# Kernel tuning notes

Measured on AMD Instinct MI355X. Metric: run time of the kernel, lower is better.

## Reference

```python
import jax, jax.numpy as jnp
import numpy as np

DEPTH, HEADS, DIM, DIM_HEAD, MLP = 2, 8, 512, 64, 2048
INNER = HEADS * DIM_HEAD  # == DIM here, but project_out is still True since dim_head != dim
NEG = -1e9


def _ln(t, g, b):
    mu = t.mean(-1, keepdims=True)
    var = ((t - mu) ** 2).mean(-1, keepdims=True)
    return (t - mu) / jnp.sqrt(var + 1e-5) * g + b


def _heads(t):
    b, n, hd = t.shape
    return t.reshape(b, n, HEADS, hd // HEADS).transpose(0, 2, 1, 3)  # b h n d


def _merge(t):
    b, h, n, d = t.shape
    return t.transpose(0, 2, 1, 3).reshape(b, n, h * d)


def kat_forward(x, kx, rd, clst, mask, kmask,
                ln1_g, ln1_b, Wqkv, Wout, bout, ln2_g, ln2_b, W1, b1, W2, b2):
    scale = DIM_HEAD ** -0.5
    # att_mask[b,1,n,m]: True where attention is disallowed (mask_i * kmask_j < 0.5)
    att_mask = (jnp.einsum('bid,bjd->bij', mask, kmask) < 0.5)[:, None]
    krd = rd[:, None]                      # [b,1,m,n]
    krdT = jnp.swapaxes(krd, -1, -2)       # [b,1,n,m]
    keep = (kmask >= 0.5)                  # kernel_mask fill-with-0 complement
    k_reps, atten = [], []
    for l in range(DEPTH):
        # pre-norm applied in-place before residual (as in the original)
        xn = _ln(x, ln1_g[l], ln1_b[l])
        kxn = _ln(kx, ln1_g[l], ln1_b[l])
        cn = _ln(clst, ln1_g[l], ln1_b[l])

        def qkv(t):
            q, k, v = jnp.split(t @ Wqkv[l], 3, axis=-1)
            return _heads(q), _heads(k), _heads(v)

        tq, tk, tv = qkv(xn)
        kq, kk, kv = qkv(kxn)
        cq, _, _ = qkv(cn)

        # patch -> kernel attention, krd-weighted dual softmax
        dots = jnp.einsum('bhid,bhjd->bhij', tq, kk) * scale      # [b,h,n,m]
        dots = jnp.where(att_mask, NEG, dots)
        attn_t = jax.nn.softmax(dots * 24, -1) * krdT             # temperature branch (attention map out)
        attn = jax.nn.softmax(dots, -1) * krdT
        x_ = _merge(jnp.einsum('bhij,bhjd->bhid', attn, kv)) @ Wout[l] + bout[l]

        # kernel -> patch attention
        kd = jnp.einsum('bhid,bhjd->bhij', kq, tk) * scale        # [b,h,m,n]
        kd = jnp.where(jnp.swapaxes(att_mask, -1, -2), NEG, kd)
        kattn = jax.nn.softmax(kd, -1) * krd
        kx_ = _merge(jnp.einsum('bhij,bhjd->bhid', kattn, tv)) @ Wout[l] + bout[l]

        # class token -> kernel attention
        cd = jnp.einsum('bhid,bhjd->bhij', cq, kk) * scale        # [b,h,1,m]
        cd = jnp.where(att_mask[:, :, :1], NEG, cd)
        c_ = _merge(jnp.einsum('bhij,bhjd->bhid', jax.nn.softmax(cd, -1), kv)) @ Wout[l] + bout[l]

        x, kx, clst = xn + x_, kxn + kx_, cn + c_

        def ff(t):
            tn = _ln(t, ln2_g[l], ln2_b[l])
            return jax.nn.gelu(tn @ W1[l] + b1[l], approximate=False) @ W2[l] + b2[l]

        x, kx, clst = ff(x) + x, ff(kx) + kx, ff(clst) + clst
        k_reps.append(kx * keep)
        atten.append(jnp.swapaxes(attn_t, -1, -2))  # [b,h,m,n]
    return jnp.stack(k_reps), clst, jnp.stack(atten)


def setup_inputs() -> dict:
    key = jax.random.key(0)
    ks = jax.random.split(key, 16)
    b, n, m = 4, 2048, 256
    s = 0.02
    L = DEPTH
    return {
        'x': jax.random.normal(ks[0], (b, n, DIM), jnp.float32),
        'kx': jax.random.normal(ks[1], (b, m, DIM), jnp.float32),
        'rd': jax.random.uniform(ks[2], (b, m, n), jnp.float32),
        'clst': jax.random.normal(ks[3], (b, 1, DIM), jnp.float32),
        'mask': jnp.ones((b, n, 1), jnp.float32),
        'kmask': jax.random.uniform(ks[4], (b, m, 1), jnp.float32),
        'ln1_g': jnp.ones((L, DIM), jnp.float32),
        'ln1_b': jnp.zeros((L, DIM), jnp.float32),
        'Wqkv': s * jax.random.normal(ks[5], (L, DIM, 3 * INNER), jnp.float32),
        'Wout': s * jax.random.normal(ks[6], (L, INNER, DIM), jnp.float32),
        'bout': jnp.zeros((L, DIM), jnp.float32),
        'ln2_g': jnp.ones((L, DIM), jnp.float32),
        'ln2_b': jnp.zeros((L, DIM), jnp.float32),
        'W1': s * jax.random.normal(ks[7], (L, DIM, MLP), jnp.float32),
        'b1': jnp.zeros((L, MLP), jnp.float32),
        'W2': s * jax.random.normal(ks[8], (L, MLP, DIM), jnp.float32),
        'b2': jnp.zeros((L, DIM), jnp.float32),
    }


def reference(x, kx, rd, clst, mask, kmask, ln1_g, ln1_b, Wqkv, Wout, bout,
              ln2_g, ln2_b, W1, b1, W2, b2):
    return kat_forward(x, kx, rd, clst, mask, kmask, ln1_g, ln1_b, Wqkv, Wout,
                       bout, ln2_g, ln2_b, W1, b1, W2, b2)
```

## Files before the change

kernel.cpp:

```cpp
#include <hip/hip_runtime.h>
#include <hip/hip_bf16.h>
#include <cstddef>

#define DEV __device__ __forceinline__

constexpr int Bb  = 4;
constexpr int Nn  = 2048;
constexpr int MK  = 256;
constexpr int Dd  = 512;
constexpr int Hh  = 8;
constexpr int DH  = 64;
constexpr int QLD = 1536;
constexpr int MLPD = 2048;
constexpr int NTOK = Bb * Nn + Bb * MK + Bb;
constexpr int KXOFF = Bb * Nn;
constexpr int CLOFF = Bb * Nn + Bb * MK;
constexpr float SCALE = 0.125f;
constexpr float NEGV  = -1e9f;

typedef __attribute__((ext_vector_type(8))) short short8;
typedef __attribute__((ext_vector_type(4))) float f32x4;

DEV float4 ldf4(const float* p) { return *reinterpret_cast<const float4*>(p); }

DEV void gload16(const short* g, short* l) {
  __builtin_amdgcn_global_load_lds(
      (const __attribute__((address_space(1))) void*)g,
      (__attribute__((address_space(3))) void*)l, 16, 0, 0);
}

DEV float waveMax(float v) {
#pragma unroll
  for (int o = 32; o; o >>= 1) v = fmaxf(v, __shfl_xor(v, o));
  return v;
}
DEV float waveSum(float v) {
#pragma unroll
  for (int o = 32; o; o >>= 1) v += __shfl_xor(v, o);
  return v;
}
DEV float blockMax256(float v, float* red) {
  v = waveMax(v);
  __syncthreads();
  if ((threadIdx.x & 63) == 0) red[threadIdx.x >> 6] = v;
  __syncthreads();
  return fmaxf(fmaxf(red[0], red[1]), fmaxf(red[2], red[3]));
}
DEV float blockSum256(float v, float* red) {
  v = waveSum(v);
  __syncthreads();
  if ((threadIdx.x & 63) == 0) red[threadIdx.x >> 6] = v;
  __syncthreads();
  return red[0] + red[1] + red[2] + red[3];
}
DEV float gelu_f(float x) { return 0.5f * x * (1.f + erff(x * 0.70710678118654752f)); }
DEV float pow24(float e1) {
  float e2 = e1 * e1, e4 = e2 * e2, e8 = e4 * e4, e16 = e8 * e8;
  return e16 * e8;
}

__global__ __launch_bounds__(256)
void copy3_kernel(const float* __restrict__ x, const float* __restrict__ kx,
                  const float* __restrict__ c, float* __restrict__ dst) {
  const int idx = blockIdx.x * 256 + threadIdx.x;
  const int row = idx >> 7;
  float4 v;
  if (row < KXOFF) v = ldf4(x + (size_t)idx * 4);
  else if (row < CLOFF) v = ldf4(kx + (size_t)idx * 4 - (size_t)KXOFF * Dd);
  else v = ldf4(c + (size_t)idx * 4 - (size_t)CLOFF * Dd);
  *reinterpret_cast<float4*>(dst + (size_t)idx * 4) = v;
}

__global__ __launch_bounds__(64)
void ln_kernel(const float* __restrict__ in, const float* __restrict__ gw,
               const float* __restrict__ bw, __hip_bfloat16* __restrict__ outb) {
  const int row = blockIdx.x;
  const int t = threadIdx.x;
  const float* p = in + (size_t)row * Dd + t * 8;
  float4 v0 = ldf4(p), v1 = ldf4(p + 4);
  float s = v0.x + v0.y + v0.z + v0.w + v1.x + v1.y + v1.z + v1.w;
  float q = v0.x*v0.x + v0.y*v0.y + v0.z*v0.z + v0.w*v0.w
          + v1.x*v1.x + v1.y*v1.y + v1.z*v1.z + v1.w*v1.w;
  s = waveSum(s); q = waveSum(q);
  const float mu = s * (1.f / Dd);
  const float rstd = rsqrtf(fmaxf(q * (1.f / Dd) - mu * mu, 0.f) + 1e-5f);
  float4 g0 = ldf4(gw + t * 8), g1 = ldf4(gw + t * 8 + 4);
  float4 b0 = ldf4(bw + t * 8), b1 = ldf4(bw + t * 8 + 4);
  float o[8];
  o[0] = (v0.x - mu) * rstd * g0.x + b0.x;
  o[1] = (v0.y - mu) * rstd * g0.y + b0.y;
  o[2] = (v0.z - mu) * rstd * g0.z + b0.z;
  o[3] = (v0.w - mu) * rstd * g0.w + b0.w;
  o[4] = (v1.x - mu) * rstd * g1.x + b1.x;
  o[5] = (v1.y - mu) * rstd * g1.y + b1.y;
  o[6] = (v1.z - mu) * rstd * g1.z + b1.z;
  o[7] = (v1.w - mu) * rstd * g1.w + b1.w;
  __hip_bfloat16* ob = outb + (size_t)row * Dd + t * 8;
#pragma unroll
  for (int e = 0; e < 8; ++e) ob[e] = __float2bfloat16(o[e]);
}

struct GArgs {
  const short* A;  long asb; int lda;
  const short* Bt; long bsb; int ldb;
  float* C; __hip_bfloat16* Cb;
  long czo, czi; int ldc;
  const float* bias;
  const float* res; const __hip_bfloat16* resb; int ldr;
  int M, N, K;
};

template<int BM, int BN, int EPI>
__global__ __launch_bounds__(256)
void mgemm(GArgs g) {
  constexpr int WMW = (BN >= 128) ? 2 : 4;
  constexpr int WNW = 4 / WMW;
  constexpr int WM = BM / WMW, WN = BN / WNW;
  constexpr int FM = WM / 16, FN = WN / 16;
  __shared__ __align__(16) short As[BM * 64];
  __shared__ __align__(16) short Bs[BN * 64];
  const int tid = threadIdx.x, l = tid & 63, w = tid >> 6;
  const int wm = (WNW == 2) ? (w >> 1) : w;
  const int wn = (WNW == 2) ? (w & 1) : 0;
  int bx = blockIdx.x, by = blockIdx.y;
  {
    const int gx = gridDim.x, nwg = gx * gridDim.y;
    const int orig = by * gx + bx;
    const int xcd = orig & 7, pos = orig >> 3;
    const int q = nwg >> 3, rmd = nwg & 7;
    const int s = (xcd < rmd ? xcd * (q + 1) : rmd * (q + 1) + (xcd - rmd) * q) + pos;
    bx = s % gx; by = s / gx;
  }
  const int z = blockIdx.z;
  const short* Ab = g.A + (size_t)z * g.asb;
  const short* Bb_ = g.Bt + (size_t)z * g.bsb;
  f32x4 acc[FM][FN] = {};
  const int lr = l & 15, lg = l >> 4;

  for (int k0 = 0; k0 < g.K; k0 += 64) {
    __syncthreads();
#pragma unroll
    for (int it = 0; it < BM / 32; ++it) {
      int idx = tid + it * 256, r = idx >> 3, c = idx & 7;
      int gm = by * BM + r;
      if (gm >= g.M) gm = g.M - 1;
      gload16(Ab + (size_t)gm * g.lda + k0 + ((c ^ (r & 7)) * 8), As + idx * 8);
    }
#pragma unroll
    for (int it = 0; it < BN / 32; ++it) {
      int idx = tid + it * 256, r = idx >> 3, c = idx & 7;
      int gn = bx * BN + r;
      gload16(Bb_ + (size_t)gn * g.ldb + k0 + ((c ^ (r & 7)) * 8), Bs + idx * 8);
    }
    __syncthreads();
#pragma unroll
    for (int ks = 0; ks < 2; ++ks) {
      short8 a[FM], b[FN];
#pragma unroll
      for (int fm = 0; fm < FM; ++fm) {
        int rr = wm * WM + fm * 16 + lr;
        int ch = (ks * 4 + lg) ^ (rr & 7);
        a[fm] = *reinterpret_cast<const short8*>(As + rr * 64 + ch * 8);
      }
#pragma unroll
      for (int fn = 0; fn < FN; ++fn) {
        int rn = wn * WN + fn * 16 + lr;
        int ch = (ks * 4 + lg) ^ (rn & 7);
        b[fn] = *reinterpret_cast<const short8*>(Bs + rn * 64 + ch * 8);
      }
#pragma unroll
      for (int fm = 0; fm < FM; ++fm)
#pragma unroll
        for (int fn = 0; fn < FN; ++fn)
          acc[fm][fn] = __builtin_amdgcn_mfma_f32_16x16x32_bf16(a[fm], b[fn], acc[fm][fn], 0, 0, 0);
    }
  }

  const size_t zoff = (size_t)(z >> 3) * g.czo + (size_t)(z & 7) * g.czi;
#pragma unroll
  for (int fm = 0; fm < FM; ++fm) {
#pragma unroll
    for (int fn = 0; fn < FN; ++fn) {
#pragma unroll
      for (int r = 0; r < 4; ++r) {
        int m = by * BM + wm * WM + fm * 16 + lg * 4 + r;
        int n = bx * BN + wn * WN + fn * 16 + lr;
        if (m >= g.M) continue;
        float v = acc[fm][fn][r];
        size_t coff = zoff + (size_t)m * g.ldc + n;
        if (EPI == 0) {
          g.C[coff] = v;
        } else if (EPI == 2) {
          v += g.bias[n] + g.res[(size_t)m * g.ldr + n];
          g.C[coff] = v;
        } else if (EPI == 5) {
          v += g.bias[n] + __bfloat162float(g.resb[(size_t)m * g.ldr + n]);
          g.C[coff] = v;
        } else if (EPI == 3) {
          v = gelu_f(v + g.bias[n]);
          g.Cb[coff] = __float2bfloat16(v);
        } else {
          g.Cb[coff] = __float2bfloat16(v);
        }
      }
    }
  }
}

template<int BM, int BN, int EPI>
static void launch_mgemm(const GArgs& g, int zdim, hipStream_t s) {
  dim3 grid((g.N + BN - 1) / BN, (g.M + BM - 1) / BM, zdim);
  mgemm<BM, BN, EPI><<<grid, 256, 0, s>>>(g);
}

__global__ __launch_bounds__(256)
void prep_attn_kernel(const float* __restrict__ qkv_x, const float* __restrict__ qkv_k,
                      __hip_bfloat16* __restrict__ tq_s, __hip_bfloat16* __restrict__ tk_hi,
                      __hip_bfloat16* __restrict__ kq_hi, __hip_bfloat16* __restrict__ kk_s,
                      __hip_bfloat16* __restrict__ tvT, __hip_bfloat16* __restrict__ kvT) {
  __shared__ float t[64][65];
  const int blk = blockIdx.x, tid = threadIdx.x;
  if (blk < 4096 + 512) {
    const bool isX = blk < 4096;
    const int T = isX ? Nn : MK;
    const float* qkv = isX ? qkv_x : qkv_k;
    const int idx = (isX ? blk : blk - 4096) * 256 + tid;
    const int token = idx >> 7, c8 = (idx & 127) * 8;
    const int b = token / T, i = token - b * T;
    const float* p = qkv + (size_t)token * QLD + c8;
    float v[8];
    float4 a = ldf4(p), c = ldf4(p + 4);
    v[0]=a.x; v[1]=a.y; v[2]=a.z; v[3]=a.w; v[4]=c.x; v[5]=c.y; v[6]=c.z; v[7]=c.w;
    if (c8 < 512) {
      int h = c8 >> 6, d = c8 & 63;
      if (isX) {
        __hip_bfloat16* q = tq_s + ((size_t)((b * 8 + h) * T + i)) * 128 + d;
#pragma unroll
        for (int e = 0; e < 8; ++e) {
          __hip_bfloat16 hi = __float2bfloat16(v[e]);
          q[e] = hi;
          q[64 + e] = __float2bfloat16(v[e] - __bfloat162float(hi));
        }
      } else {
        __hip_bfloat16* q = kq_hi + ((size_t)((b * 8 + h) * T + i)) * 64 + d;
#pragma unroll
        for (int e = 0; e < 8; ++e) q[e] = __float2bfloat16(v[e]);
      }
    } else {
      int cc = c8 - 512, h = cc >> 6, d = cc & 63;
      if (isX) {
        __hip_bfloat16* k = tk_hi + ((size_t)((b * 8 + h) * T + i)) * 64 + d;
#pragma unroll
        for (int e = 0; e < 8; ++e) k[e] = __float2bfloat16(v[e]);
      } else {
        __hip_bfloat16* k = kk_s + ((size_t)((b * 8 + h) * T + i)) * 128 + d;
#pragma unroll
        for (int e = 0; e < 8; ++e) {
          __hip_bfloat16 hi = __float2bfloat16(v[e]);
          k[e] = hi;
          k[64 + e] = __float2bfloat16(v[e] - __bfloat162float(hi));
        }
      }
    }
    return;
  }
  const bool isX = blk < 5632;
  const int r = isX ? blk - 4608 : blk - 5632;
  const int T = isX ? Nn : MK;
  const int tilesPerBh = T / 64;
  const int bh = r / tilesPerBh, i0 = (r % tilesPerBh) * 64;
  const int b = bh >> 3, h = bh & 7;
  const float* qkv = isX ? qkv_x : qkv_k;
  __hip_bfloat16* vT = isX ? tvT : kvT;
#pragma unroll
  for (int it = 0; it < 4; ++it) {
    int idx = tid + it * 256, rr = idx >> 4, f = idx & 15;
    float4 v = ldf4(qkv + (size_t)(b * T + i0 + rr) * QLD + 2 * Dd + h * 64 + f * 4);
    t[rr][f * 4 + 0] = v.x; t[rr][f * 4 + 1] = v.y;
    t[rr][f * 4 + 2] = v.z; t[rr][f * 4 + 3] = v.w;
  }
  __syncthreads();
#pragma unroll
  for (int it = 0; it < 4; ++it) {
    int idx = tid + it * 256, d = idx >> 4, c4 = (idx & 15) * 4;
    __hip_bfloat16* op = vT + (size_t)(bh * 64 + d) * T + i0 + c4;
#pragma unroll
    for (int e = 0; e < 4; ++e) op[e] = __float2bfloat16(t[c4 + e][d]);
  }
}

__global__ __launch_bounds__(512)
void score_sx_kernel(const short* __restrict__ Q, const short* __restrict__ Km,
                     const float* __restrict__ mask, const float* __restrict__ kmask,
                     const float* __restrict__ rdT,
                     __hip_bfloat16* __restrict__ P1, float* __restrict__ atten) {
  __shared__ __align__(16) char smem[49152];
  short* As = (short*)smem;
  short* Bs = (short*)(smem + 16384);
  float* tb = (float*)smem;
  __shared__ float red[128 * 2];
  __shared__ float red2[128 * 4];
  const int tid = threadIdx.x, l = tid & 63, w = tid >> 6;
  const int wm = w >> 1, wn = w & 1;
  const int by = blockIdx.x, bh = blockIdx.y;
  const int b = bh >> 3;
  const short* Ab = Q + (size_t)bh * Nn * 128;
  const short* Bb = Km + (size_t)bh * MK * 128;
  const int lr = l & 15, lg = l >> 4;
  f32x4 acc[2][8] = {};

  for (int k0 = 0; k0 < 128; k0 += 64) {
    __syncthreads();
#pragma unroll
    for (int it = 0; it < 2; ++it) {
      int idx = tid + it * 512, r = idx >> 3, c = idx & 7;
      gload16(Ab + (size_t)(by * 128 + r) * 128 + k0 + ((c ^ (r & 7)) * 8), As + idx * 8);
    }
#pragma unroll
    for (int it = 0; it < 4; ++it) {
      int idx = tid + it * 512, r = idx >> 3, c = idx & 7;
      gload16(Bb + (size_t)r * 128 + k0 + ((c ^ (r & 7)) * 8), Bs + idx * 8);
    }
    __syncthreads();
#pragma unroll
    for (int ks = 0; ks < 2; ++ks) {
      short8 a[2], bv[8];
#pragma unroll
      for (int fm = 0; fm < 2; ++fm) {
        int rr = wm * 32 + fm * 16 + lr;
        int ch = (ks * 4 + lg) ^ (rr & 7);
        a[fm] = *reinterpret_cast<const short8*>(As + rr * 64 + ch * 8);
      }
#pragma unroll
      for (int fn = 0; fn < 8; ++fn) {
        int rn = wn * 128 + fn * 16 + lr;
        int ch = (ks * 4 + lg) ^ (rn & 7);
        bv[fn] = *reinterpret_cast<const short8*>(Bs + rn * 64 + ch * 8);
      }
#pragma unroll
      for (int fm = 0; fm < 2; ++fm)
#pragma unroll
        for (int fn = 0; fn < 8; ++fn)
          acc[fm][fn] = __builtin_amdgcn_mfma_f32_16x16x32_bf16(a[fm], bv[fn], acc[fm][fn], 0, 0, 0);
    }
  }
  {
    float colm[8];
#pragma unroll
    for (int fn = 0; fn < 8; ++fn)
      colm[fn] = kmask[b * MK + wn * 128 + fn * 16 + lr];
#pragma unroll
    for (int fm = 0; fm < 2; ++fm)
#pragma unroll
      for (int r = 0; r < 4; ++r) {
        float rm = mask[(size_t)b * Nn + by * 128 + wm * 32 + fm * 16 + lg * 4 + r];
#pragma unroll
        for (int fn = 0; fn < 8; ++fn)
          acc[fm][fn][r] = (rm * colm[fn] < 0.5f) ? NEGV : acc[fm][fn][r] * SCALE;
      }
  }
  float mx[2][4];
#pragma unroll
  for (int fm = 0; fm < 2; ++fm)
#pragma unroll
    for (int r = 0; r < 4; ++r) {
      float m = -3.4e38f;
#pragma unroll
      for (int fn = 0; fn < 8; ++fn) m = fmaxf(m, acc[fm][fn][r]);
#pragma unroll
      for (int o = 8; o; o >>= 1) m = fmaxf(m, __shfl_xor(m, o));
      mx[fm][r] = m;
    }
  __syncthreads();
  if (lr == 0) {
#pragma unroll
    for (int fm = 0; fm < 2; ++fm)
#pragma unroll
      for (int r = 0; r < 4; ++r)
        red[(wm * 32 + fm * 16 + lg * 4 + r) * 2 + wn] = mx[fm][r];
  }
  __syncthreads();
#pragma unroll
  for (int fm = 0; fm < 2; ++fm)
#pragma unroll
    for (int r = 0; r < 4; ++r) {
      int row = wm * 32 + fm * 16 + lg * 4 + r;
      mx[fm][r] = fmaxf(red[row * 2], red[row * 2 + 1]);
    }
  float s1[2][4], s24[2][4];
#pragma unroll
  for (int fm = 0; fm < 2; ++fm)
#pragma unroll
    for (int r = 0; r < 4; ++r) {
      float a1 = 0.f, a24 = 0.f;
#pragma unroll
      for (int fn = 0; fn < 8; ++fn) {
        float e1 = __expf(acc[fm][fn][r] - mx[fm][r]);
        acc[fm][fn][r] = e1;
        a1 += e1;
        a24 += pow24(e1);
      }
#pragma unroll
      for (int o = 8; o; o >>= 1) { a1 += __shfl_xor(a1, o); a24 += __shfl_xor(a24, o); }
      s1[fm][r] = a1; s24[fm][r] = a24;
    }
  __syncthreads();
  if (lr == 0) {
#pragma unroll
    for (int fm = 0; fm < 2; ++fm)
#pragma unroll
      for (int r = 0; r < 4; ++r) {
        int row = wm * 32 + fm * 16 + lg * 4 + r;
        red2[row * 4 + wn * 2]     = s1[fm][r];
        red2[row * 4 + wn * 2 + 1] = s24[fm][r];
      }
  }
  __syncthreads();
#pragma unroll
  for (int fm = 0; fm < 2; ++fm)
#pragma unroll
    for (int r = 0; r < 4; ++r) {
      int row = wm * 32 + fm * 16 + lg * 4 + r;
      s1[fm][r]  = 1.f / (red2[row * 4] + red2[row * 4 + 2]);
      s24[fm][r] = 1.f / (red2[row * 4 + 1] + red2[row * 4 + 3]);
    }
#pragma unroll
  for (int fm = 0; fm < 2; ++fm) {
#pragma unroll
    for (int r = 0; r < 4; ++r) {
      int m = by * 128 + wm * 32 + fm * 16 + lg * 4 + r;
      const float* rp = rdT + ((size_t)b * Nn + m) * MK;
      size_t obase = ((size_t)bh * Nn + m) * MK;
#pragma unroll
      for (int fn = 0; fn < 8; ++fn) {
        int n = wn * 128 + fn * 16 + lr;
        float e1 = acc[fm][fn][r];
        float rv = rp[n];
        P1[obase + n] = __float2bfloat16(e1 * s1[fm][r] * rv);
        acc[fm][fn][r] = pow24(e1) * s24[fm][r] * rv;
      }
    }
  }
  const int jw = tid >> 1, ipw = (tid & 1) * 16;
#pragma unroll
  for (int c = 0; c < 4; ++c) {
    __syncthreads();
    if (wm == c) {
#pragma unroll
      for (int fm = 0; fm < 2; ++fm)
#pragma unroll
        for (int r = 0; r < 4; ++r) {
          int mloc = fm * 16 + lg * 4 + r;
#pragma unroll
          for (int fn = 0; fn < 8; ++fn) {
            int n = wn * 128 + fn * 16 + lr;
            tb[n * 33 + mloc] = acc[fm][fn][r];
          }
        }
    }
    __syncthreads();
    float* op = atten + ((size_t)bh * MK + jw) * Nn + by * 128 + c * 32 + ipw;
    const float* tp = tb + jw * 33 + ipw;
#pragma unroll
    for (int e = 0; e < 4; ++e)
      *reinterpret_cast<float4*>(op + e * 4) =
          make_float4(tp[e * 4], tp[e * 4 + 1], tp[e * 4 + 2], tp[e * 4 + 3]);
  }
}

__global__ __launch_bounds__(256)
void score_sk_kernel(const short* __restrict__ Qk, const short* __restrict__ Kt,
                     const float* __restrict__ mask, const float* __restrict__ kmask,
                     const float* __restrict__ rd, __hip_bfloat16* __restrict__ P2) {
  __shared__ __align__(16) short As[16 * 64];
  __shared__ __align__(16) short Bs[256 * 64];
  __shared__ float redm[16 * 4];
  __shared__ float reds[16 * 4];
  const int tid = threadIdx.x, l = tid & 63, w = tid >> 6;
  const int lr = l & 15, lg = l >> 4;
  const int bh = blockIdx.x, j0 = blockIdx.y * 16, b = bh >> 3;
  const short* Ab = Qk + ((size_t)bh * MK + j0) * 64;
  const short* Bb = Kt + (size_t)bh * Nn * 64;
  f32x4 acc[32];
#pragma unroll
  for (int q = 0; q < 32; ++q) acc[q] = f32x4{0.f, 0.f, 0.f, 0.f};
  if (tid < 128) {
    int r = tid >> 3, c = tid & 7;
    gload16(Ab + (size_t)r * 64 + ((c ^ (r & 7)) * 8), As + tid * 8);
  }
#pragma unroll
  for (int nc = 0; nc < 8; ++nc) {
    __syncthreads();
#pragma unroll
    for (int it = 0; it < 8; ++it) {
      int idx = tid + it * 256, r = idx >> 3, c = idx & 7;
      gload16(Bb + (size_t)(nc * 256 + r) * 64 + ((c ^ (r & 7)) * 8), Bs + idx * 8);
    }
    __syncthreads();
#pragma unroll
    for (int ks = 0; ks < 2; ++ks) {
      short8 a;
      {
        int ch = (ks * 4 + lg) ^ (lr & 7);
        a = *reinterpret_cast<const short8*>(As + lr * 64 + ch * 8);
      }
#pragma unroll
      for (int fn = 0; fn < 4; ++fn) {
        int rn = w * 64 + fn * 16 + lr;
        int ch = (ks * 4 + lg) ^ (rn & 7);
        short8 bv = *reinterpret_cast<const short8*>(Bs + rn * 64 + ch * 8);
        acc[nc * 4 + fn] =
            __builtin_amdgcn_mfma_f32_16x16x32_bf16(a, bv, acc[nc * 4 + fn], 0, 0, 0);
      }
    }
  }
  float rm[4];
#pragma unroll
  for (int rr = 0; rr < 4; ++rr) rm[rr] = kmask[b * MK + j0 + lg * 4 + rr];
  float mx[4] = {-3.4e38f, -3.4e38f, -3.4e38f, -3.4e38f};
#pragma unroll
  for (int q = 0; q < 32; ++q) {
    int n = (q >> 2) * 256 + w * 64 + (q & 3) * 16 + lr;
    float cm = mask[(size_t)b * Nn + n];
#pragma unroll
    for (int rr = 0; rr < 4; ++rr) {
      float v = (rm[rr] * cm < 0.5f) ? NEGV : acc[q][rr] * SCALE;
      acc[q][rr] = v;
      mx[rr] = fmaxf(mx[rr], v);
    }
  }
#pragma unroll
  for (int o = 8; o; o >>= 1)
#pragma unroll
    for (int rr = 0; rr < 4; ++rr) mx[rr] = fmaxf(mx[rr], __shfl_xor(mx[rr], o));
  __syncthreads();
  if (lr == 0) {
#pragma unroll
    for (int rr = 0; rr < 4; ++rr) redm[(lg * 4 + rr) * 4 + w] = mx[rr];
  }
  __syncthreads();
#pragma unroll
  for (int rr = 0; rr < 4; ++rr) {
    int row = lg * 4 + rr;
    mx[rr] = fmaxf(fmaxf(redm[row * 4], redm[row * 4 + 1]),
                   fmaxf(redm[row * 4 + 2], redm[row * 4 + 3]));
  }
  float sm[4] = {0.f, 0.f, 0.f, 0.f};
#pragma unroll
  for (int q = 0; q < 32; ++q)
#pragma unroll
    for (int rr = 0; rr < 4; ++rr) {
      float e = __expf(acc[q][rr] - mx[rr]);
      acc[q][rr] = e;
      sm[rr] += e;
    }
#pragma unroll
  for (int o = 8; o; o >>= 1)
#pragma unroll
    for (int rr = 0; rr < 4; ++rr) sm[rr] += __shfl_xor(sm[rr], o);
  __syncthreads();
  if (lr == 0) {
#pragma unroll
    for (int rr = 0; rr < 4; ++rr) reds[(lg * 4 + rr) * 4 + w] = sm[rr];
  }
  __syncthreads();
  float inv[4];
#pragma unroll
  for (int rr = 0; rr < 4; ++rr) {
    int row = lg * 4 + rr;
    inv[rr] = 1.f / (reds[row * 4] + reds[row * 4 + 1] + reds[row * 4 + 2] + reds[row * 4 + 3]);
  }
#pragma unroll
  for (int rr = 0; rr < 4; ++rr) {
    int j = j0 + lg * 4 + rr;
    const float* rp = rd + (size_t)(b * MK + j) * Nn;
    __hip_bfloat16* pp = P2 + ((size_t)bh * MK + j) * Nn;
#pragma unroll
    for (int q = 0; q < 32; ++q) {
      int n = (q >> 2) * 256 + w * 64 + (q & 3) * 16 + lr;
      pp[n] = __float2bfloat16(acc[q][rr] * inv[rr] * rp[n]);
    }
  }
}

__global__ __launch_bounds__(256)
void rd_tr_kernel(const float* __restrict__ rd, float* __restrict__ rdT) {
  __shared__ float tb[64][65];
  const int b = blockIdx.x;
  const int i0 = blockIdx.y * 64, j0 = blockIdx.z * 64;
  const int tid = threadIdx.x;
#pragma unroll
  for (int it = 0; it < 4; ++it) {
    int idx = tid + it * 256, r = idx >> 4, c4 = (idx & 15) * 4;
    float4 v = ldf4(rd + ((size_t)(b * MK + j0 + r)) * Nn + i0 + c4);
    tb[r][c4 + 0] = v.x; tb[r][c4 + 1] = v.y; tb[r][c4 + 2] = v.z; tb[r][c4 + 3] = v.w;
  }
  __syncthreads();
#pragma unroll
  for (int it = 0; it < 4; ++it) {
    int idx = tid + it * 256, r = idx >> 4, c4 = (idx & 15) * 4;
    float4 o = make_float4(tb[c4 + 0][r], tb[c4 + 1][r], tb[c4 + 2][r], tb[c4 + 3][r]);
    *reinterpret_cast<float4*>(rdT + ((size_t)(b * Nn + i0 + r)) * MK + j0 + c4) = o;
  }
}

struct WtArgs {
  const float* W[8];
  __hip_bfloat16* T[8];
  int K[8], N[8];
};
__global__ __launch_bounds__(256)
void wtrans_all_kernel(WtArgs a) {
  __shared__ float t[64][65];
  const int e = blockIdx.z;
  const int K = a.K[e], N = a.N[e];
  const int n0 = blockIdx.x * 64, k0 = blockIdx.y * 64;
  if (n0 >= N || k0 >= K) return;
  const float* W = a.W[e];
  __hip_bfloat16* WT = a.T[e];
  const int tid = threadIdx.x;
#pragma unroll
  for (int it = 0; it < 4; ++it) {
    int idx = tid + it * 256, r = idx >> 4, f = idx & 15;
    float4 v = ldf4(W + (size_t)(k0 + r) * N + n0 + f * 4);
    t[r][f * 4 + 0] = v.x; t[r][f * 4 + 1] = v.y;
    t[r][f * 4 + 2] = v.z; t[r][f * 4 + 3] = v.w;
  }
  __syncthreads();
#pragma unroll
  for (int it = 0; it < 4; ++it) {
    int idx = tid + it * 256, r = idx >> 4, c4 = (idx & 15) * 4;
    __hip_bfloat16* op = WT + (size_t)(n0 + r) * K + k0 + c4;
#pragma unroll
    for (int e2 = 0; e2 < 4; ++e2) op[e2] = __float2bfloat16(t[c4 + e2][r]);
  }
}

__global__ __launch_bounds__(256)
void attn_c_kernel(const float* __restrict__ cqkv, const float* __restrict__ kqkv,
                   const float* __restrict__ mask, const float* __restrict__ kmask,
                   __hip_bfloat16* __restrict__ c_pre) {
  __shared__ __align__(16) float kv_s[MK][DH];
  __shared__ __align__(16) float q_s[DH];
  __shared__ float pbuf[MK];
  __shared__ float red8[8];
  __shared__ float redpv[4][DH];
  const int tid = threadIdx.x;
  const int bh = blockIdx.x, b = bh >> 3, h = bh & 7;
  const float* vp = kqkv + ((size_t)(b * MK + tid)) * QLD + 2 * Dd + h * DH;
#pragma unroll
  for (int q4 = 0; q4 < 16; ++q4)
    *reinterpret_cast<float4*>(&kv_s[tid][q4 * 4]) = ldf4(vp + q4 * 4);
  if (tid < DH) q_s[tid] = cqkv[(size_t)b * QLD + h * DH + tid];
  __syncthreads();
  const float* kp = kqkv + ((size_t)(b * MK + tid)) * QLD + Dd + h * DH;
  float dot = 0.f;
#pragma unroll
  for (int q4 = 0; q4 < 16; ++q4) {
    float4 kv4 = ldf4(kp + q4 * 4);
    float4 qv = ldf4(&q_s[q4 * 4]);
    dot = fmaf(qv.x, kv4.x, dot);
    dot = fmaf(qv.y, kv4.y, dot);
    dot = fmaf(qv.z, kv4.z, dot);
    dot = fmaf(qv.w, kv4.w, dot);
  }
  const float dm = (mask[(size_t)b * Nn] * kmask[b * MK + tid] < 0.5f) ? NEGV : dot * SCALE;
  const float mx = blockMax256(dm, red8);
  const float e = __expf(dm - mx);
  const float s = blockSum256(e, red8);
  pbuf[tid] = e / s;
  __syncthreads();
  const int d = tid & 63, g = tid >> 6;
  float acc = 0.f;
#pragma unroll 8
  for (int jj = 0; jj < 64; ++jj)
    acc = fmaf(pbuf[g * 64 + jj], kv_s[g * 64 + jj][d], acc);
  redpv[g][d] = acc;
  __syncthreads();
  if (tid < DH)
    c_pre[(size_t)b * Dd + h * DH + tid] = __float2bfloat16(
        redpv[0][tid] + redpv[1][tid] + redpv[2][tid] + redpv[3][tid]);
}

__global__ void kreps_kernel(const float* __restrict__ kx, const float* __restrict__ kmask,
                             float* __restrict__ o) {
  const int idx = blockIdx.x * 256 + threadIdx.x;
  const int bj = idx >> 9;
  const float keep = (kmask[bj] >= 0.5f) ? 1.f : 0.f;
  o[idx] = kx[idx] * keep;
}
__global__ void cout_kernel(const float* __restrict__ c_s, float* __restrict__ o) {
  const int idx = blockIdx.x * 256 + threadIdx.x;
  o[idx] = c_s[idx];
}

static GArgs ga_base() { GArgs g = {}; return g; }

extern "C" void kernel_launch(void* const* d_in, const int* in_sizes, int n_in,
                              void* d_out, int out_size, void* d_ws, size_t ws_size,
                              hipStream_t stream) {
  (void)in_sizes; (void)n_in; (void)out_size; (void)ws_size;
  const float* x_in  = (const float*)d_in[0];
  const float* kx_in = (const float*)d_in[1];
  const float* rd    = (const float*)d_in[2];
  const float* c_in  = (const float*)d_in[3];
  const float* mask  = (const float*)d_in[4];
  const float* kmask = (const float*)d_in[5];
  const float* ln1g  = (const float*)d_in[6];
  const float* ln1b  = (const float*)d_in[7];
  const float* Wqkv  = (const float*)d_in[8];
  const float* Woutw = (const float*)d_in[9];
  const float* boutw = (const float*)d_in[10];
  const float* ln2g  = (const float*)d_in[11];
  const float* ln2b  = (const float*)d_in[12];
  const float* W1    = (const float*)d_in[13];
  const float* b1    = (const float*)d_in[14];
  const float* W2    = (const float*)d_in[15];
  const float* b2    = (const float*)d_in[16];
  float* out = (float*)d_out;

  float* ws = (float*)d_ws;
  size_t off = 0;
  auto alloc = [&](size_t n) { float* p = ws + off; off += (n + 15) & ~(size_t)15; return p; };
  float* xcat_s    = alloc((size_t)NTOK * Dd);
  float* xcat_nb_f = alloc((size_t)NTOK * Dd / 2);
  float* pre_cat_f = alloc((size_t)NTOK * Dd / 2);
  float* qkv       = alloc((size_t)NTOK * QLD);
  float* P1_f      = alloc((size_t)32 * Nn * MK / 2);
  float* P2_f      = alloc((size_t)32 * MK * Nn / 2);
  float* tq_s_f    = alloc((size_t)32 * Nn * 128 / 2);
  float* kk_s_f    = alloc((size_t)32 * MK * 128 / 2);
  float* tk_hi_f   = alloc((size_t)32 * Nn * 64 / 2);
  float* kq_hi_f   = alloc((size_t)32 * MK * 64 / 2);
  float* tvT_f     = alloc((size_t)32 * 64 * Nn / 2);
  float* kvT_f     = alloc((size_t)32 * 64 * MK / 2);
  float* rdT       = alloc((size_t)Bb * Nn * MK);
  float* WqkvT_f   = alloc((size_t)2 * QLD * Dd / 2);
  float* WoutT_f   = alloc((size_t)2 * Dd * Dd / 2);
  float* W1T_f     = alloc((size_t)2 * MLPD * Dd / 2);
  float* W2T_f     = alloc((size_t)2 * Dd * MLPD / 2);

  __hip_bfloat16* xcat_nb = (__hip_bfloat16*)xcat_nb_f;
  __hip_bfloat16* pre_cat = (__hip_bfloat16*)pre_cat_f;
  __hip_bfloat16* P1b     = (__hip_bfloat16*)P1_f;
  __hip_bfloat16* P2b     = (__hip_bfloat16*)P2_f;
  __hip_bfloat16* tq_s    = (__hip_bfloat16*)tq_s_f;
  __hip_bfloat16* kk_s    = (__hip_bfloat16*)kk_s_f;
  __hip_bfloat16* tk_hi   = (__hip_bfloat16*)tk_hi_f;
  __hip_bfloat16* kq_hi   = (__hip_bfloat16*)kq_hi_f;
  __hip_bfloat16* tvT     = (__hip_bfloat16*)tvT_f;
  __hip_bfloat16* kvT     = (__hip_bfloat16*)kvT_f;
  __hip_bfloat16* WqkvT   = (__hip_bfloat16*)WqkvT_f;
  __hip_bfloat16* WoutT   = (__hip_bfloat16*)WoutT_f;
  __hip_bfloat16* W1T     = (__hip_bfloat16*)W1T_f;
  __hip_bfloat16* W2T     = (__hip_bfloat16*)W2T_f;
  __hip_bfloat16* hid     = (__hip_bfloat16*)qkv;

  const size_t CL_OFF = (size_t)2 * Bb * MK * Dd;
  const size_t AT_OFF = CL_OFF + (size_t)Bb * Dd;

  copy3_kernel<<<(NTOK * 128) / 256, 256, 0, stream>>>(x_in, kx_in, c_in, xcat_s);
  rd_tr_kernel<<<dim3(Bb, Nn / 64, MK / 64), 256, 0, stream>>>(rd, rdT);
  {
    WtArgs a;
    for (int l = 0; l < 2; ++l) {
      a.W[l * 4 + 0] = Wqkv + (size_t)l * Dd * QLD;  a.T[l * 4 + 0] = WqkvT + (size_t)l * QLD * Dd;
      a.K[l * 4 + 0] = Dd;   a.N[l * 4 + 0] = QLD;
      a.W[l * 4 + 1] = Woutw + (size_t)l * Dd * Dd;  a.T[l * 4 + 1] = WoutT + (size_t)l * Dd * Dd;
      a.K[l * 4 + 1] = Dd;   a.N[l * 4 + 1] = Dd;
      a.W[l * 4 + 2] = W1 + (size_t)l * Dd * MLPD;   a.T[l * 4 + 2] = W1T + (size_t)l * MLPD * Dd;
      a.K[l * 4 + 2] = Dd;   a.N[l * 4 + 2] = MLPD;
      a.W[l * 4 + 3] = W2 + (size_t)l * MLPD * Dd;   a.T[l * 4 + 3] = W2T + (size_t)l * Dd * MLPD;
      a.K[l * 4 + 3] = MLPD; a.N[l * 4 + 3] = Dd;
    }
    wtrans_all_kernel<<<dim3(32, 32, 8), 256, 0, stream>>>(a);
  }

  for (int l = 0; l < 2; ++l) {
    const float* bo  = boutw + (size_t)l * Dd;
    const float* b1l = b1 + (size_t)l * MLPD;
    const float* b2l = b2 + (size_t)l * Dd;
    __hip_bfloat16* WqkvTl = WqkvT + (size_t)l * QLD * Dd;
    __hip_bfloat16* WoutTl = WoutT + (size_t)l * Dd * Dd;
    __hip_bfloat16* W1Tl   = W1T + (size_t)l * MLPD * Dd;
    __hip_bfloat16* W2Tl   = W2T + (size_t)l * Dd * MLPD;

    ln_kernel<<<NTOK, 64, 0, stream>>>(xcat_s, ln1g + l * Dd, ln1b + l * Dd, xcat_nb);

    {
      GArgs g = ga_base();
      g.A = (const short*)xcat_nb; g.lda = Dd;
      g.Bt = (const short*)WqkvTl; g.ldb = Dd;
      g.C = qkv; g.ldc = QLD;
      g.M = NTOK; g.N = QLD; g.K = Dd;
      launch_mgemm<128, 128, 0>(g, 1, stream);
    }

    prep_attn_kernel<<<5760, 256, 0, stream>>>(
        qkv, qkv + (size_t)KXOFF * QLD, tq_s, tk_hi, kq_hi, kk_s, tvT, kvT);

    attn_c_kernel<<<Bb * Hh, 256, 0, stream>>>(qkv + (size_t)CLOFF * QLD,
                                               qkv + (size_t)KXOFF * QLD, mask, kmask,
                                               pre_cat + (size_t)CLOFF * Dd);

    score_sx_kernel<<<dim3(Nn / 128, 32), 512, 0, stream>>>(
        (const short*)tq_s, (const short*)kk_s, mask, kmask, rdT, P1b,
        out + AT_OFF + (size_t)l * 32 * MK * Nn);
    {
      GArgs g = ga_base();
      g.A = (const short*)P1b; g.asb = (long)Nn * MK; g.lda = MK;
      g.Bt = (const short*)kvT; g.bsb = (long)64 * MK; g.ldb = MK;
      g.Cb = pre_cat; g.czo = (long)Nn * Dd; g.czi = 64; g.ldc = Dd;
      g.M = Nn; g.N = 64; g.K = MK;
      launch_mgemm<128, 64, 4>(g, 32, stream);
    }
    score_sk_kernel<<<dim3(32, MK / 16), 256, 0, stream>>>(
        (const short*)kq_hi, (const short*)tk_hi, mask, kmask, rd, P2b);
    {
      GArgs g = ga_base();
      g.A = (const short*)P2b; g.asb = (long)MK * Nn; g.lda = Nn;
      g.Bt = (const short*)tvT; g.bsb = (long)64 * Nn; g.ldb = Nn;
      g.Cb = pre_cat + (size_t)KXOFF * Dd; g.czo = (long)MK * Dd; g.czi = 64; g.ldc = Dd;
      g.M = MK; g.N = 64; g.K = Nn;
      launch_mgemm<64, 64, 4>(g, 32, stream);
    }

    {
      GArgs g = ga_base();
      g.A = (const short*)pre_cat; g.lda = Dd;
      g.Bt = (const short*)WoutTl; g.ldb = Dd;
      g.C = xcat_s; g.ldc = Dd; g.bias = bo; g.resb = xcat_nb; g.ldr = Dd;
      g.M = NTOK; g.N = Dd; g.K = Dd;
      launch_mgemm<128, 64, 5>(g, 1, stream);
    }

    ln_kernel<<<NTOK, 64, 0, stream>>>(xcat_s, ln2g + l * Dd, ln2b + l * Dd, xcat_nb);
    {
      GArgs g = ga_base();
      g.A = (const short*)xcat_nb; g.lda = Dd;
      g.Bt = (const short*)W1Tl; g.ldb = Dd;
      g.Cb = hid; g.ldc = MLPD; g.bias = b1l;
      g.M = NTOK; g.N = MLPD; g.K = Dd;
      launch_mgemm<128, 128, 3>(g, 1, stream);
      GArgs h = ga_base();
      h.A = (const short*)hid; h.lda = MLPD;
      h.Bt = (const short*)W2Tl; h.ldb = MLPD;
      h.C = xcat_s; h.ldc = Dd; h.bias = b2l; h.res = xcat_s; h.ldr = Dd;
      h.M = NTOK; h.N = Dd; h.K = MLPD;
      launch_mgemm<128, 64, 2>(h, 1, stream);
    }

    kreps_kernel<<<(Bb * MK * Dd) / 256, 256, 0, stream>>>(
        xcat_s + (size_t)KXOFF * Dd, kmask, out + (size_t)l * Bb * MK * Dd);
  }
  cout_kernel<<<(Bb * Dd) / 256, 256, 0, stream>>>(xcat_s + (size_t)CLOFF * Dd, out + CL_OFF);
}
```

Baseline: 687.9 us.

## Fuse QKV projection with attention-layout scatter and fold kernel-rep output into MLP epilogue

Replaces the generic QKV GEMM plus separate prep_attn relayout kernel with a dedicated GEMM whose epilogue writes bf16 hi/lo split Q/K, transposed V via shared memory, and the class-token query directly. This avoids writing and rereading the full fp32 qkv buffer. The class-token attention now reads the bf16 split K and transposed V. The masked kernel-rep output is produced in the W2 GEMM epilogue instead of a separate kernel. The cost is scattered epilogue stores and slightly different precision on the class-token path.

New measurement: 653.2 us, median of 2. -5.1%, faster.

```diff
diff --git a/kernel.cpp b/kernel.cpp
--- a/kernel.cpp
+++ b/kernel.cpp
@@ -57,6 +57,10 @@
 DEV float pow24(float e1) {
   float e2 = e1 * e1, e4 = e2 * e2, e8 = e4 * e4, e16 = e8 * e8;
   return e16 * e8;
+}
+DEV short bf16bits(float v) {
+  __hip_bfloat16 h = __float2bfloat16(v);
+  return *reinterpret_cast<short*>(&h);
 }
 
 __global__ __launch_bounds__(256)
@@ -107,6 +111,7 @@
   long czo, czi; int ldc;
   const float* bias;
   const float* res; const __hip_bfloat16* resb; int ldr;
+  float* out2; const float* km2;
   int M, N, K;
 };
 
@@ -196,6 +201,14 @@
         } else if (EPI == 5) {
           v += g.bias[n] + __bfloat162float(g.resb[(size_t)m * g.ldr + n]);
           g.C[coff] = v;
+        } else if (EPI == 6) {
+          v += g.bias[n] + g.res[(size_t)m * g.ldr + n];
+          g.C[coff] = v;
+          if (m >= KXOFF && m < CLOFF) {
+            int t = m - KXOFF;
+            float keep = (g.km2[t] >= 0.5f) ? 1.f : 0.f;
+            g.out2[(size_t)t * Dd + n] = v * keep;
+          }
         } else if (EPI == 3) {
           v = gelu_f(v + g.bias[n]);
           g.Cb[coff] = __float2bfloat16(v);
@@ -213,79 +226,159 @@
   mgemm<BM, BN, EPI><<<grid, 256, 0, s>>>(g);
 }
 
+struct QArgs {
+  const short* A; int lda;
+  const short* Bt; int ldb;
+  __hip_bfloat16 *tq, *tk, *kq, *kk, *tvT, *kvT;
+  float* cq;
+  int M, K;
+};
+
 __global__ __launch_bounds__(256)
-void prep_attn_kernel(const float* __restrict__ qkv_x, const float* __restrict__ qkv_k,
-                      __hip_bfloat16* __restrict__ tq_s, __hip_bfloat16* __restrict__ tk_hi,
-                      __hip_bfloat16* __restrict__ kq_hi, __hip_bfloat16* __restrict__ kk_s,
-                      __hip_bfloat16* __restrict__ tvT, __hip_bfloat16* __restrict__ kvT) {
-  __shared__ float t[64][65];
-  const int blk = blockIdx.x, tid = threadIdx.x;
-  if (blk < 4096 + 512) {
-    const bool isX = blk < 4096;
-    const int T = isX ? Nn : MK;
-    const float* qkv = isX ? qkv_x : qkv_k;
-    const int idx = (isX ? blk : blk - 4096) * 256 + tid;
-    const int token = idx >> 7, c8 = (idx & 127) * 8;
-    const int b = token / T, i = token - b * T;
-    const float* p = qkv + (size_t)token * QLD + c8;
-    float v[8];
-    float4 a = ldf4(p), c = ldf4(p + 4);
-    v[0]=a.x; v[1]=a.y; v[2]=a.z; v[3]=a.w; v[4]=c.x; v[5]=c.y; v[6]=c.z; v[7]=c.w;
-    if (c8 < 512) {
-      int h = c8 >> 6, d = c8 & 63;
-      if (isX) {
-        __hip_bfloat16* q = tq_s + ((size_t)((b * 8 + h) * T + i)) * 128 + d;
-#pragma unroll
-        for (int e = 0; e < 8; ++e) {
-          __hip_bfloat16 hi = __float2bfloat16(v[e]);
-          q[e] = hi;
-          q[64 + e] = __float2bfloat16(v[e] - __bfloat162float(hi));
+void qkv_gemm(QArgs g) {
+  __shared__ __align__(16) char smem[34816];
+  short* As = (short*)smem;
+  short* Bs = (short*)(smem + 16384);
+  short* tb = (short*)smem;
+  const int tid = threadIdx.x, l = tid & 63, w = tid >> 6;
+  const int wm = w >> 1, wn = w & 1;
+  int bx = blockIdx.x, by = blockIdx.y;
+  {
+    const int gx = gridDim.x, nwg = gx * gridDim.y;
+    const int orig = by * gx + bx;
+    const int xcd = orig & 7, pos = orig >> 3;
+    const int q = nwg >> 3, rmd = nwg & 7;
+    const int s = (xcd < rmd ? xcd * (q + 1) : rmd * (q + 1) + (xcd - rmd) * q) + pos;
+    bx = s % gx; by = s / gx;
+  }
+  f32x4 acc[4][4] = {};
+  const int lr = l & 15, lg = l >> 4;
+
+  for (int k0 = 0; k0 < g.K; k0 += 64) {
+    __syncthreads();
+#pragma unroll
+    for (int it = 0; it < 4; ++it) {
+      int idx = tid + it * 256, r = idx >> 3, c = idx & 7;
+      int gm = by * 128 + r;
+      if (gm >= g.M) gm = g.M - 1;
+      gload16(g.A + (size_t)gm * g.lda + k0 + ((c ^ (r & 7)) * 8), As + idx * 8);
+    }
+#pragma unroll
+    for (int it = 0; it < 4; ++it) {
+      int idx = tid + it * 256, r = idx >> 3, c = idx & 7;
+      int gn = bx * 128 + r;
+      gload16(g.Bt + (size_t)gn * g.ldb + k0 + ((c ^ (r & 7)) * 8), Bs + idx * 8);
+    }
+    __syncthreads();
+#pragma unroll
+    for (int ks = 0; ks < 2; ++ks) {
+      short8 a[4], b[4];
+#pragma unroll
+      for (int fm = 0; fm < 4; ++fm) {
+        int rr = wm * 64 + fm * 16 + lr;
+        int ch = (ks * 4 + lg) ^ (rr & 7);
+        a[fm] = *reinterpret_cast<const short8*>(As + rr * 64 + ch * 8);
+      }
+#pragma unroll
+      for (int fn = 0; fn < 4; ++fn) {
+        int rn = wn * 64 + fn * 16 + lr;
+        int ch = (ks * 4 + lg) ^ (rn & 7);
+        b[fn] = *reinterpret_cast<const short8*>(Bs + rn * 64 + ch * 8);
+      }
+#pragma unroll
+      for (int fm = 0; fm < 4; ++fm)
+#pragma unroll
+        for (int fn = 0; fn < 4; ++fn)
+          acc[fm][fn] = __builtin_amdgcn_mfma_f32_16x16x32_bf16(a[fm], b[fn], acc[fm][fn], 0, 0, 0);
+    }
+  }
+
+  const int sec = bx >> 2;
+  const int region = (by < 64) ? 0 : (by < 72 ? 1 : 2);
+
+  if (sec == 2) {
+    if (region == 2) return;
+    __syncthreads();
+#pragma unroll
+    for (int fm = 0; fm < 4; ++fm)
+#pragma unroll
+      for (int fn = 0; fn < 4; ++fn)
+#pragma unroll
+        for (int r = 0; r < 4; ++r) {
+          int mloc = wm * 64 + fm * 16 + lg * 4 + r;
+          int nloc = wn * 64 + fn * 16 + lr;
+          tb[nloc * 136 + mloc] = bf16bits(acc[fm][fn][r]);
         }
-      } else {
-        __hip_bfloat16* q = kq_hi + ((size_t)((b * 8 + h) * T + i)) * 64 + d;
-#pragma unroll
-        for (int e = 0; e < 8; ++e) q[e] = __float2bfloat16(v[e]);
-      }
+    __syncthreads();
+    const int nloc = tid >> 1, mh = (tid & 1) * 64;
+    const int nv = (bx - 8) * 128 + nloc;
+    const int h = nv >> 6, d = nv & 63;
+    int T, b, ibase;
+    __hip_bfloat16* vT;
+    if (region == 0) {
+      T = Nn; b = by >> 4; ibase = (by & 15) * 128 + mh; vT = g.tvT;
     } else {
-      int cc = c8 - 512, h = cc >> 6, d = cc & 63;
-      if (isX) {
-        __hip_bfloat16* k = tk_hi + ((size_t)((b * 8 + h) * T + i)) * 64 + d;
-#pragma unroll
-        for (int e = 0; e < 8; ++e) k[e] = __float2bfloat16(v[e]);
-      } else {
-        __hip_bfloat16* k = kk_s + ((size_t)((b * 8 + h) * T + i)) * 128 + d;
-#pragma unroll
-        for (int e = 0; e < 8; ++e) {
-          __hip_bfloat16 hi = __float2bfloat16(v[e]);
-          k[e] = hi;
-          k[64 + e] = __float2bfloat16(v[e] - __bfloat162float(hi));
+      T = MK; int t0 = (by - 64) * 128 + mh; b = t0 >> 8; ibase = t0 & 255; vT = g.kvT;
+    }
+    short* dst = (short*)vT + ((size_t)(b * 8 + h) * 64 + d) * T + ibase;
+    const short* src = tb + nloc * 136 + mh;
+#pragma unroll
+    for (int e = 0; e < 8; ++e)
+      *reinterpret_cast<short8*>(dst + e * 8) = *reinterpret_cast<const short8*>(src + e * 8);
+    return;
+  }
+
+  if (region == 2) {
+    if (sec == 0) {
+#pragma unroll
+      for (int fm = 0; fm < 4; ++fm)
+#pragma unroll
+        for (int fn = 0; fn < 4; ++fn)
+#pragma unroll
+          for (int r = 0; r < 4; ++r) {
+            int m = by * 128 + wm * 64 + fm * 16 + lg * 4 + r;
+            if (m >= g.M) continue;
+            int n = bx * 128 + wn * 64 + fn * 16 + lr;
+            g.cq[(size_t)(m - CLOFF) * Dd + n] = acc[fm][fn][r];
+          }
+    }
+    return;
+  }
+
+  const int T = region ? MK : Nn;
+#pragma unroll
+  for (int fm = 0; fm < 4; ++fm) {
+#pragma unroll
+    for (int fn = 0; fn < 4; ++fn) {
+#pragma unroll
+      for (int r = 0; r < 4; ++r) {
+        int m = by * 128 + wm * 64 + fm * 16 + lg * 4 + r;
+        int n = bx * 128 + wn * 64 + fn * 16 + lr;
+        float v = acc[fm][fn][r];
+        int t = region ? m - KXOFF : m;
+        int b = region ? (t >> 8) : (t >> 11);
+        int i = region ? (t & 255) : (t & 2047);
+        int h = (n >> 6) & 7, d = n & 63;
+        size_t tok = (size_t)(b * 8 + h) * T + i;
+        if (sec == 0) {
+          if (region == 0) {
+            __hip_bfloat16 hi = __float2bfloat16(v);
+            g.tq[tok * 128 + d] = hi;
+            g.tq[tok * 128 + 64 + d] = __float2bfloat16(v - __bfloat162float(hi));
+          } else {
+            g.kq[tok * 64 + d] = __float2bfloat16(v);
+          }
+        } else {
+          if (region == 0) {
+            g.tk[tok * 64 + d] = __float2bfloat16(v);
+          } else {
+            __hip_bfloat16 hi = __float2bfloat16(v);
+            g.kk[tok * 128 + d] = hi;
+            g.kk[tok * 128 + 64 + d] = __float2bfloat16(v - __bfloat162float(hi));
+          }
         }
       }
     }
-    return;
-  }
-  const bool isX = blk < 5632;
-  const int r = isX ? blk - 4608 : blk - 5632;
-  const int T = isX ? Nn : MK;
-  const int tilesPerBh = T / 64;
-  const int bh = r / tilesPerBh, i0 = (r % tilesPerBh) * 64;
-  const int b = bh >> 3, h = bh & 7;
-  const float* qkv = isX ? qkv_x : qkv_k;
-  __hip_bfloat16* vT = isX ? tvT : kvT;
-#pragma unroll
-  for (int it = 0; it < 4; ++it) {
-    int idx = tid + it * 256, rr = idx >> 4, f = idx & 15;
-    float4 v = ldf4(qkv + (size_t)(b * T + i0 + rr) * QLD + 2 * Dd + h * 64 + f * 4);
-    t[rr][f * 4 + 0] = v.x; t[rr][f * 4 + 1] = v.y;
-    t[rr][f * 4 + 2] = v.z; t[rr][f * 4 + 3] = v.w;
-  }
-  __syncthreads();
-#pragma unroll
-  for (int it = 0; it < 4; ++it) {
-    int idx = tid + it * 256, d = idx >> 4, c4 = (idx & 15) * 4;
-    __hip_bfloat16* op = vT + (size_t)(bh * 64 + d) * T + i0 + c4;
-#pragma unroll
-    for (int e = 0; e < 4; ++e) op[e] = __float2bfloat16(t[c4 + e][d]);
   }
 }
 
@@ -637,7 +730,8 @@
 }
 
 __global__ __launch_bounds__(256)
-void attn_c_kernel(const float* __restrict__ cqkv, const float* __restrict__ kqkv,
+void attn_c_kernel(const float* __restrict__ cq, const __hip_bfloat16* __restrict__ kk,
+                   const __hip_bfloat16* __restrict__ kvT,
                    const float* __restrict__ mask, const float* __restrict__ kmask,
                    __hip_bfloat16* __restrict__ c_pre) {
   __shared__ __align__(16) float kv_s[MK][DH];
@@ -647,22 +741,17 @@
   __shared__ float redpv[4][DH];
   const int tid = threadIdx.x;
   const int bh = blockIdx.x, b = bh >> 3, h = bh & 7;
-  const float* vp = kqkv + ((size_t)(b * MK + tid)) * QLD + 2 * Dd + h * DH;
-#pragma unroll
-  for (int q4 = 0; q4 < 16; ++q4)
-    *reinterpret_cast<float4*>(&kv_s[tid][q4 * 4]) = ldf4(vp + q4 * 4);
-  if (tid < DH) q_s[tid] = cqkv[(size_t)b * QLD + h * DH + tid];
-  __syncthreads();
-  const float* kp = kqkv + ((size_t)(b * MK + tid)) * QLD + Dd + h * DH;
+#pragma unroll
+  for (int d = 0; d < DH; ++d)
+    kv_s[tid][d] = __bfloat162float(kvT[((size_t)(b * 8 + h) * 64 + d) * MK + tid]);
+  if (tid < DH) q_s[tid] = cq[(size_t)b * Dd + h * DH + tid];
+  __syncthreads();
+  const __hip_bfloat16* kp = kk + ((size_t)((b * 8 + h) * MK + tid)) * 128;
   float dot = 0.f;
 #pragma unroll
-  for (int q4 = 0; q4 < 16; ++q4) {
-    float4 kv4 = ldf4(kp + q4 * 4);
-    float4 qv = ldf4(&q_s[q4 * 4]);
-    dot = fmaf(qv.x, kv4.x, dot);
-    dot = fmaf(qv.y, kv4.y, dot);
-    dot = fmaf(qv.z, kv4.z, dot);
-    dot = fmaf(qv.w, kv4.w, dot);
+  for (int d = 0; d < DH; ++d) {
+    float kd = __bfloat162float(kp[d]) + __bfloat162float(kp[64 + d]);
+    dot = fmaf(q_s[d], kd, dot);
   }
   const float dm = (mask[(size_t)b * Nn] * kmask[b * MK + tid] < 0.5f) ? NEGV : dot * SCALE;
   const float mx = blockMax256(dm, red8);
@@ -682,13 +771,6 @@
         redpv[0][tid] + redpv[1][tid] + redpv[2][tid] + redpv[3][tid]);
 }
 
-__global__ void kreps_kernel(const float* __restrict__ kx, const float* __restrict__ kmask,
-                             float* __restrict__ o) {
-  const int idx = blockIdx.x * 256 + threadIdx.x;
-  const int bj = idx >> 9;
-  const float keep = (kmask[bj] >= 0.5f) ? 1.f : 0.f;
-  o[idx] = kx[idx] * keep;
-}
 __global__ void cout_kernel(const float* __restrict__ c_s, float* __restrict__ o) {
   const int idx = blockIdx.x * 256 + threadIdx.x;
   o[idx] = c_s[idx];
@@ -725,7 +807,8 @@
   float* xcat_s    = alloc((size_t)NTOK * Dd);
   float* xcat_nb_f = alloc((size_t)NTOK * Dd / 2);
   float* pre_cat_f = alloc((size_t)NTOK * Dd / 2);
-  float* qkv       = alloc((size_t)NTOK * QLD);
+  float* hid_f     = alloc((size_t)NTOK * MLPD / 2);
+  float* cq        = alloc((size_t)Bb * Dd);
   float* P1_f      = alloc((size_t)32 * Nn * MK / 2);
   float* P2_f      = alloc((size_t)32 * MK * Nn / 2);
   float* tq_s_f    = alloc((size_t)32 * Nn * 128 / 2);
@@ -742,6 +825,7 @@
 
   __hip_bfloat16* xcat_nb = (__hip_bfloat16*)xcat_nb_f;
   __hip_bfloat16* pre_cat = (__hip_bfloat16*)pre_cat_f;
+  __hip_bfloat16* hid     = (__hip_bfloat16*)hid_f;
   __hip_bfloat16* P1b     = (__hip_bfloat16*)P1_f;
   __hip_bfloat16* P2b     = (__hip_bfloat16*)P2_f;
   __hip_bfloat16* tq_s    = (__hip_bfloat16*)tq_s_f;
@@ -754,7 +838,6 @@
   __hip_bfloat16* WoutT   = (__hip_bfloat16*)WoutT_f;
   __hip_bfloat16* W1T     = (__hip_bfloat16*)W1T_f;
   __hip_bfloat16* W2T     = (__hip_bfloat16*)W2T_f;
-  __hip_bfloat16* hid     = (__hip_bfloat16*)qkv;
 
   const size_t CL_OFF = (size_t)2 * Bb * MK * Dd;
   const size_t AT_OFF = CL_OFF + (size_t)Bb * Dd;
@@ -788,19 +871,16 @@
     ln_kernel<<<NTOK, 64, 0, stream>>>(xcat_s, ln1g + l * Dd, ln1b + l * Dd, xcat_nb);
 
     {
-      GArgs g = ga_base();
-      g.A = (const short*)xcat_nb; g.lda = Dd;
-      g.Bt = (const short*)WqkvTl; g.ldb = Dd;
-      g.C = qkv; g.ldc = QLD;
-      g.M = NTOK; g.N = QLD; g.K = Dd;
-      launch_mgemm<128, 128, 0>(g, 1, stream);
-    }
-
-    prep_attn_kernel<<<5760, 256, 0, stream>>>(
-        qkv, qkv + (size_t)KXOFF * QLD, tq_s, tk_hi, kq_hi, kk_s, tvT, kvT);
-
-    attn_c_kernel<<<Bb * Hh, 256, 0, stream>>>(qkv + (size_t)CLOFF * QLD,
-                                               qkv + (size_t)KXOFF * QLD, mask, kmask,
+      QArgs q = {};
+      q.A = (const short*)xcat_nb; q.lda = Dd;
+      q.Bt = (const short*)WqkvTl; q.ldb = Dd;
+      q.tq = tq_s; q.tk = tk_hi; q.kq = kq_hi; q.kk = kk_s;
+      q.tvT = tvT; q.kvT = kvT; q.cq = cq;
+      q.M = NTOK; q.K = Dd;
+      qkv_gemm<<<dim3(QLD / 128, (NTOK + 127) / 128, 1), 256, 0, stream>>>(q);
+    }
+
+    attn_c_kernel<<<Bb * Hh, 256, 0, stream>>>(cq, kk_s, kvT, mask, kmask,
                                                pre_cat + (size_t)CLOFF * Dd);
 
     score_sx_kernel<<<dim3(Nn / 128, 32), 512, 0, stream>>>(
@@ -846,12 +926,10 @@
       h.A = (const short*)hid; h.lda = MLPD;
       h.Bt = (const short*)W2Tl; h.ldb = MLPD;
       h.C = xcat_s; h.ldc = Dd; h.bias = b2l; h.res = xcat_s; h.ldr = Dd;
+      h.out2 = out + (size_t)l * Bb * MK * Dd; h.km2 = kmask;
       h.M = NTOK; h.N = Dd; h.K = MLPD;
-      launch_mgemm<128, 64, 2>(h, 1, stream);
-    }
-
-    kreps_kernel<<<(Bb * MK * Dd) / 256, 256, 0, stream>>>(
-        xcat_s + (size_t)KXOFF * Dd, kmask, out + (size_t)l * Bb * MK * Dd);
+      launch_mgemm<128, 64, 6>(h, 1, stream);
+    }
   }
   cout_kernel<<<(Bb * Dd) / 256, 256, 0, stream>>>(xcat_s + (size_t)CLOFF * Dd, out + CL_OFF);
 }
```
